# Kernel optimization log

Measured on AMD Instinct MI355X. Metric: run time of the kernel, lower is better.

Reference implementation:

```python
import jax, jax.numpy as jnp
import numpy as np


def setup_inputs() -> dict:
    key = jax.random.key(0)
    ks = jax.random.split(key, 8)
    N, D, DC, H, C = 100000, 1024, 512, 256, 2  # instances, feat, compressed, hidden, classes
    s = lambda k, sh: jax.random.normal(k, sh, dtype=jnp.float32) * 0.02
    return {
        "x": jax.random.normal(ks[0], (N, D), dtype=jnp.float32),
        "Wc": s(ks[1], (D, DC)), "bc": jnp.zeros((DC,), jnp.float32),
        "W1": s(ks[2], (D, H)), "b1": jnp.zeros((H,), jnp.float32),
        "W2": s(ks[3], (D, H)), "b2": jnp.zeros((H,), jnp.float32),
        "W3": s(ks[4], (H, C)), "b3": jnp.zeros((C,), jnp.float32),
        "Wbag": s(ks[5], (DC, 1)), "bbag": jnp.zeros((1,), jnp.float32),
        "Wins": s(ks[6], (DC, C)), "bins": jnp.zeros((C,), jnp.float32),
        "bag_label": 1,
        "n_ins": 8,
    }


def reference(x, Wc, bc, W1, b1, W2, b2, W3, b3, Wbag, bbag, Wins, bins, bag_label, n_ins):
    # G_Att_Net: compression + gated attention (vectorized over the per-instance loop)
    h = jax.nn.relu(x @ Wc + bc)                                  # [N, 512]
    a = jnp.tanh(x @ W1 + b1) * jax.nn.sigmoid(x @ W2 + b2)       # [N, 256] gated
    A = a @ W3 + b3                                               # [N, n_class]

    # Bag.h_slide: sum_i A[i]^T @ h[i]  ==  A^T @ h
    slide_agg_rep = A.T @ h                                       # [n_class, 512]
    slide_score_unnorm = (slide_agg_rep @ Wbag + bbag).reshape(1, -1)  # [1, n_class]
    Y_prob = jax.nn.softmax(slide_score_unnorm, axis=-1)
    Y_hat = jnp.argmax(slide_score_unnorm, axis=-1)

    # Ins.in_call: top-k positive / negative instances on attention column bag_label
    A_I = A[:, bag_label]                                         # [N]
    _, pos_idx = jax.lax.top_k(A_I, n_ins)
    _, neg_idx = jax.lax.top_k(-A_I, n_ins)
    ins_in = h[jnp.concatenate([pos_idx, neg_idx])]               # [2*n_ins, 512]
    ins_logits = jax.nn.softmax(ins_in @ Wins + bins, axis=-1)    # [2*n_ins, n_class]
    ins_labels = jnp.concatenate([jnp.ones((n_ins,), jnp.int32),
                                  jnp.zeros((n_ins,), jnp.int32)])
    return slide_score_unnorm, Y_hat, Y_prob, ins_logits, ins_labels
```

## Files before the change

### kernel.cpp

```cpp
#include <hip/hip_runtime.h>
#include <hip/hip_bf16.h>
#include <math.h>

typedef __attribute__((ext_vector_type(8))) short bf16x8;
typedef __attribute__((ext_vector_type(4))) float f32x4;

#define M_ROWS 100000
#define NBLK   1563

static __device__ __forceinline__ unsigned short f2bf(float f) {
  union { float f; unsigned u; } cv; cv.f = f;
  unsigned u = cv.u;
  return (unsigned short)((u + 0x7fffu + ((u >> 16) & 1u)) >> 16);
}

static __device__ __forceinline__ f32x4 mfma16(bf16x8 a, bf16x8 b, f32x4 c) {
  return __builtin_amdgcn_mfma_f32_16x16x32_bf16(a, b, c, 0, 0, 0);
}

static __device__ __forceinline__ void gload_lds16(const unsigned short* g, unsigned short* l) {
  __builtin_amdgcn_global_load_lds((const __attribute__((address_space(1))) unsigned int*)g,
                                   (__attribute__((address_space(3))) unsigned int*)l, 16, 0, 0);
}

__global__ void prep_kernel(const float* __restrict__ Wc, const float* __restrict__ W1,
                            const float* __restrict__ W2,
                            unsigned short* __restrict__ Wct, unsigned short* __restrict__ W1t,
                            unsigned short* __restrict__ W2t, float* __restrict__ agg1) {
  int i = blockIdx.x * blockDim.x + threadIdx.x;
  if (i < 1024) agg1[i] = 0.0f;
  if (i < 512 * 1024) {
    int c = i >> 10, k = i & 1023;
    Wct[i] = f2bf(Wc[k * 512 + c]);
  } else if (i < 768 * 1024) {
    int j = i - 512 * 1024;
    int c = j >> 10, k = j & 1023;
    W1t[j] = f2bf(W1[k * 256 + c]);
  } else if (i < 1024 * 1024) {
    int j = i - 768 * 1024;
    int c = j >> 10, k = j & 1023;
    W2t[j] = f2bf(W2[k * 256 + c]);
  }
}

__launch_bounds__(512)
__global__ void kernelA(const float* __restrict__ x,
                        const unsigned short* __restrict__ W1t, const unsigned short* __restrict__ W2t,
                        const float* __restrict__ b1, const float* __restrict__ b2,
                        const float* __restrict__ W3, const float* __restrict__ b3,
                        float* __restrict__ Ag) {
  __shared__ unsigned short xl[64 * 32];
  __shared__ unsigned short w1l[256 * 32];
  __shared__ unsigned short w2l[256 * 32];
  __shared__ float Alds[64 * 2];

  const int tid = threadIdx.x;
  const int lane = tid & 63, wid = tid >> 6;
  const int wm = wid >> 2, wj = wid & 3;
  const int lr = lane & 15, lg = lane >> 4;
  const int m0 = blockIdx.x * 64;

  f32x4 acc1[2][4], acc2[2][4];
#pragma unroll
  for (int m = 0; m < 2; m++)
#pragma unroll
    for (int n = 0; n < 4; n++) {
      acc1[m][n] = (f32x4){0.f, 0.f, 0.f, 0.f};
      acc2[m][n] = (f32x4){0.f, 0.f, 0.f, 0.f};
    }

  const int xr = tid >> 3;
  const bool xvalid = (m0 + xr) < M_ROWS;
  const float* xsrc = x + (size_t)(m0 + xr) * 1024 + ((tid & 7) << 2);
  unsigned short* xdst = &xl[tid * 4];

  const unsigned short* w1base = W1t + (size_t)(wid * 16 + (lane >> 2)) * 1024 + ((lane & 3) << 3);
  const unsigned short* w2base = W2t + (size_t)(wid * 16 + (lane >> 2)) * 1024 + ((lane & 3) << 3);
  unsigned short* w1dst0 = &w1l[wid * 512];
  unsigned short* w1dst1 = &w1l[4096 + wid * 512];
  unsigned short* w2dst0 = &w2l[wid * 512];
  unsigned short* w2dst1 = &w2l[4096 + wid * 512];

  const bf16x8* ap0 = (const bf16x8*)&xl[(wm * 32 + 0 + lr) * 32 + lg * 8];
  const bf16x8* ap1 = (const bf16x8*)&xl[(wm * 32 + 16 + lr) * 32 + lg * 8];
  const bf16x8* b1p[4]; const bf16x8* b2p[4];
#pragma unroll
  for (int n = 0; n < 4; n++) {
    b1p[n] = (const bf16x8*)&w1l[(wj * 64 + n * 16 + lr) * 32 + lg * 8];
    b2p[n] = (const bf16x8*)&w2l[(wj * 64 + n * 16 + lr) * 32 + lg * 8];
  }

  for (int ks = 0; ks < 32; ks++) {
    const int k0 = ks * 32;
    gload_lds16(w1base + k0, w1dst0);
    gload_lds16(w1base + 131072 + k0, w1dst1);
    gload_lds16(w2base + k0, w2dst0);
    gload_lds16(w2base + 131072 + k0, w2dst1);
    float4 xv = make_float4(0.f, 0.f, 0.f, 0.f);
    if (xvalid) xv = *(const float4*)(xsrc + k0);
    ushort4 xb;
    xb.x = f2bf(xv.x); xb.y = f2bf(xv.y); xb.z = f2bf(xv.z); xb.w = f2bf(xv.w);
    *(ushort4*)xdst = xb;
    __syncthreads();
    bf16x8 a0 = *ap0, a1 = *ap1;
#pragma unroll
    for (int n = 0; n < 4; n++) {
      bf16x8 bb1 = *b1p[n];
      acc1[0][n] = mfma16(a0, bb1, acc1[0][n]);
      acc1[1][n] = mfma16(a1, bb1, acc1[1][n]);
      bf16x8 bb2 = *b2p[n];
      acc2[0][n] = mfma16(a0, bb2, acc2[0][n]);
      acc2[1][n] = mfma16(a1, bb2, acc2[1][n]);
    }
    __syncthreads();
  }

  float pA[2][4][2];
#pragma unroll
  for (int m = 0; m < 2; m++)
#pragma unroll
    for (int r = 0; r < 4; r++) { pA[m][r][0] = 0.f; pA[m][r][1] = 0.f; }

#pragma unroll
  for (int n = 0; n < 4; n++) {
    const int j = wj * 64 + n * 16 + lr;
    const float bb1 = b1[j], bb2 = b2[j];
    const float w30 = W3[j * 2], w31 = W3[j * 2 + 1];
#pragma unroll
    for (int m = 0; m < 2; m++)
#pragma unroll
      for (int r = 0; r < 4; r++) {
        float u1 = acc1[m][n][r] + bb1;
        float u2 = acc2[m][n][r] + bb2;
        float av = tanhf(u1) * (1.0f / (1.0f + __expf(-u2)));
        pA[m][r][0] += av * w30;
        pA[m][r][1] += av * w31;
      }
  }
#pragma unroll
  for (int off = 1; off < 16; off <<= 1)
#pragma unroll
    for (int m = 0; m < 2; m++)
#pragma unroll
      for (int r = 0; r < 4; r++) {
        pA[m][r][0] += __shfl_xor(pA[m][r][0], off, 64);
        pA[m][r][1] += __shfl_xor(pA[m][r][1], off, 64);
      }

  if (tid < 128) Alds[tid] = 0.0f;
  __syncthreads();
  if (lr == 0) {
#pragma unroll
    for (int m = 0; m < 2; m++)
#pragma unroll
      for (int r = 0; r < 4; r++) {
        int row = wm * 32 + m * 16 + lg * 4 + r;
        atomicAdd(&Alds[row * 2 + 0], pA[m][r][0]);
        atomicAdd(&Alds[row * 2 + 1], pA[m][r][1]);
      }
  }
  __syncthreads();
  if (tid < 128) {
    int row = tid >> 1, c = tid & 1;
    if (m0 + row < M_ROWS) Ag[(size_t)(m0 + row) * 2 + c] = Alds[tid] + b3[c];
  }
}

template <bool MIN>
static __device__ __forceinline__ bool better(float v1, int i1, float v2, int i2) {
  if (MIN) return (v1 < v2) || (v1 == v2 && i1 < i2);
  else     return (v1 > v2) || (v1 == v2 && i1 < i2);
}

template <bool MIN>
static __device__ __forceinline__ void merge_lists(float* vL, int* iL, int t, int s) {
  float av[8], ov[8], mv[8];
  int ai[8], oi[8], mi[8];
#pragma unroll
  for (int p = 0; p < 8; p++) {
    av[p] = vL[t * 8 + p];       ai[p] = iL[t * 8 + p];
    ov[p] = vL[(t + s) * 8 + p]; oi[p] = iL[(t + s) * 8 + p];
  }
#pragma unroll
  for (int p = 0; p < 8; p++) {
    bool b = better<MIN>(av[p], ai[p], ov[7 - p], oi[7 - p]);
    mv[p] = b ? av[p] : ov[7 - p];
    mi[p] = b ? ai[p] : oi[7 - p];
  }
#define CE(i, j)                                                             \
  { if (!better<MIN>(mv[i], mi[i], mv[j], mi[j])) {                          \
      float tv = mv[i]; mv[i] = mv[j]; mv[j] = tv;                           \
      int tii = mi[i]; mi[i] = mi[j]; mi[j] = tii; } }
  CE(0, 4) CE(1, 5) CE(2, 6) CE(3, 7)
  CE(0, 2) CE(1, 3) CE(4, 6) CE(5, 7)
  CE(0, 1) CE(2, 3) CE(4, 5) CE(6, 7)
#undef CE
#pragma unroll
  for (int p = 0; p < 8; p++) { vL[t * 8 + p] = mv[p]; iL[t * 8 + p] = mi[p]; }
}

__launch_bounds__(256)
__global__ void topk_p1(const float* __restrict__ Ag, const int* __restrict__ bag_label,
                        float* __restrict__ tkv, int* __restrict__ tki,
                        float* __restrict__ bkv, int* __restrict__ bki) {
  __shared__ float tvL[256 * 8]; __shared__ int tiL[256 * 8];
  __shared__ float bvL[256 * 8]; __shared__ int biL[256 * 8];
  const int t = threadIdx.x;
  const int lab = bag_label[0];
  float tv[8], bv[8]; int ti[8], bi[8];
#pragma unroll
  for (int p = 0; p < 8; p++) {
    tv[p] = -3.4e38f; ti[p] = 0x7fffffff;
    bv[p] =  3.4e38f; bi[p] = 0x7fffffff;
  }
  for (int r = blockIdx.x * 256 + t; r < M_ROWS; r += 65536) {
    float v = Ag[(size_t)r * 2 + lab];
    {
      float cv = v; int ci = r;
#pragma unroll
      for (int p = 0; p < 8; p++) {
        bool b = (cv > tv[p]) || (cv == tv[p] && ci < ti[p]);
        if (b) { float t0 = tv[p]; int t1 = ti[p]; tv[p] = cv; ti[p] = ci; cv = t0; ci = t1; }
      }
    }
    {
      float cv = v; int ci = r;
#pragma unroll
      for (int p = 0; p < 8; p++) {
        bool b = (cv < bv[p]) || (cv == bv[p] && ci < bi[p]);
        if (b) { float t0 = bv[p]; int t1 = bi[p]; bv[p] = cv; bi[p] = ci; cv = t0; ci = t1; }
      }
    }
  }
#pragma unroll
  for (int p = 0; p < 8; p++) {
    tvL[t * 8 + p] = tv[p]; tiL[t * 8 + p] = ti[p];
    bvL[t * 8 + p] = bv[p]; biL[t * 8 + p] = bi[p];
  }
  __syncthreads();
  for (int s = 128; s > 0; s >>= 1) {
    if (t < s) {
      merge_lists<false>(tvL, tiL, t, s);
      merge_lists<true>(bvL, biL, t, s);
    }
    __syncthreads();
  }
  if (t < 8) {
    tkv[blockIdx.x * 8 + t] = tvL[t]; tki[blockIdx.x * 8 + t] = tiL[t];
    bkv[blockIdx.x * 8 + t] = bvL[t]; bki[blockIdx.x * 8 + t] = biL[t];
  }
}

__launch_bounds__(256)
__global__ void topk_p2(const float* __restrict__ tkv, const int* __restrict__ tki,
                        const float* __restrict__ bkv, const int* __restrict__ bki,
                        int* __restrict__ idxout, float* __restrict__ out) {
  __shared__ float tvL[256 * 8]; __shared__ int tiL[256 * 8];
  __shared__ float bvL[256 * 8]; __shared__ int biL[256 * 8];
  const int t = threadIdx.x;
#pragma unroll
  for (int p = 0; p < 8; p++) {
    tvL[t * 8 + p] = tkv[t * 8 + p]; tiL[t * 8 + p] = tki[t * 8 + p];
    bvL[t * 8 + p] = bkv[t * 8 + p]; biL[t * 8 + p] = bki[t * 8 + p];
  }
  __syncthreads();
  for (int s = 128; s > 0; s >>= 1) {
    if (t < s) {
      merge_lists<false>(tvL, tiL, t, s);
      merge_lists<true>(bvL, biL, t, s);
    }
    __syncthreads();
  }
  if (t == 0) {
#pragma unroll
    for (int p = 0; p < 8; p++) {
      idxout[p] = tiL[p];
      idxout[8 + p] = biL[p];
      out[37 + p] = 1.0f;
      out[45 + p] = 0.0f;
    }
  }
}

__launch_bounds__(512)
__global__ void kernelH(const float* __restrict__ x,
                        const unsigned short* __restrict__ Wct,
                        const float* __restrict__ bc,
                        const float* __restrict__ Ag,
                        const int* __restrict__ idx,
                        float* __restrict__ aggP,
                        float* __restrict__ hsel) {
  __shared__ unsigned short xl[64 * 32];
  __shared__ unsigned short wl[512 * 32];
  __shared__ float aggL[1024];
  __shared__ int selr[16];

  const int tid = threadIdx.x;
  const int lane = tid & 63, wid = tid >> 6;
  const int wm = wid >> 2, wc = wid & 3;
  const int lr = lane & 15, lg = lane >> 4;
  const int m0 = blockIdx.x * 64;

  f32x4 acc[2][8];
#pragma unroll
  for (int m = 0; m < 2; m++)
#pragma unroll
    for (int n = 0; n < 8; n++) acc[m][n] = (f32x4){0.f, 0.f, 0.f, 0.f};

  const int xr = tid >> 3;
  const bool xvalid = (m0 + xr) < M_ROWS;
  const float* xsrc = x + (size_t)(m0 + xr) * 1024 + ((tid & 7) << 2);
  unsigned short* xdst = &xl[tid * 4];

  const unsigned short* wbase = Wct + (size_t)(wid * 16 + (lane >> 2)) * 1024 + ((lane & 3) << 3);
  unsigned short* wdst0 = &wl[wid * 512];
  unsigned short* wdst1 = &wl[4096 + wid * 512];
  unsigned short* wdst2 = &wl[8192 + wid * 512];
  unsigned short* wdst3 = &wl[12288 + wid * 512];

  const bf16x8* ap0 = (const bf16x8*)&xl[(wm * 32 + 0 + lr) * 32 + lg * 8];
  const bf16x8* ap1 = (const bf16x8*)&xl[(wm * 32 + 16 + lr) * 32 + lg * 8];
  const bf16x8* bp[8];
#pragma unroll
  for (int n = 0; n < 8; n++)
    bp[n] = (const bf16x8*)&wl[(wc * 128 + n * 16 + lr) * 32 + lg * 8];

  for (int ks = 0; ks < 32; ks++) {
    const int k0 = ks * 32;
    gload_lds16(wbase + k0, wdst0);
    gload_lds16(wbase + 131072 + k0, wdst1);
    gload_lds16(wbase + 262144 + k0, wdst2);
    gload_lds16(wbase + 393216 + k0, wdst3);
    float4 xv = make_float4(0.f, 0.f, 0.f, 0.f);
    if (xvalid) xv = *(const float4*)(xsrc + k0);
    ushort4 xb;
    xb.x = f2bf(xv.x); xb.y = f2bf(xv.y); xb.z = f2bf(xv.z); xb.w = f2bf(xv.w);
    *(ushort4*)xdst = xb;
    __syncthreads();
    bf16x8 a0 = *ap0, a1 = *ap1;
#pragma unroll
    for (int n = 0; n < 8; n++) {
      bf16x8 bb = *bp[n];
      acc[0][n] = mfma16(a0, bb, acc[0][n]);
      acc[1][n] = mfma16(a1, bb, acc[1][n]);
    }
    __syncthreads();
  }

  if (tid < 16) {
    int r = idx[tid];
    selr[tid] = (r >= m0 && r < m0 + 64) ? (r - m0) : -1;
  }
  aggL[tid] = 0.0f;
  aggL[tid + 512] = 0.0f;
  __syncthreads();

  float av[2][4][2];
#pragma unroll
  for (int m = 0; m < 2; m++)
#pragma unroll
    for (int r = 0; r < 4; r++) {
      int row = m0 + wm * 32 + m * 16 + lg * 4 + r;
      bool valid = row < M_ROWS;
      av[m][r][0] = valid ? Ag[(size_t)row * 2 + 0] : 0.f;
      av[m][r][1] = valid ? Ag[(size_t)row * 2 + 1] : 0.f;
    }

  float contrib[8][2];
#pragma unroll
  for (int n = 0; n < 8; n++) { contrib[n][0] = 0.f; contrib[n][1] = 0.f; }

#pragma unroll
  for (int n = 0; n < 8; n++) {
    const float bcv = bc[wc * 128 + n * 16 + lr];
#pragma unroll
    for (int m = 0; m < 2; m++)
#pragma unroll
      for (int r = 0; r < 4; r++) {
        float h = fmaxf(acc[m][n][r] + bcv, 0.0f);
        acc[m][n][r] = h;
        contrib[n][0] += av[m][r][0] * h;
        contrib[n][1] += av[m][r][1] * h;
      }
  }
#pragma unroll
  for (int n = 0; n < 8; n++)
#pragma unroll
    for (int c = 0; c < 2; c++) {
      contrib[n][c] += __shfl_xor(contrib[n][c], 16, 64);
      contrib[n][c] += __shfl_xor(contrib[n][c], 32, 64);
    }
  if (lg == 0) {
#pragma unroll
    for (int n = 0; n < 8; n++) {
      atomicAdd(&aggL[wc * 128 + n * 16 + lr], contrib[n][0]);
      atomicAdd(&aggL[512 + wc * 128 + n * 16 + lr], contrib[n][1]);
    }
  }
#pragma unroll
  for (int s = 0; s < 16; s++) {
    int rl = selr[s];
    if (rl < 0 || (rl >> 5) != wm) continue;
#pragma unroll
    for (int m = 0; m < 2; m++)
#pragma unroll
      for (int r = 0; r < 4; r++)
        if (rl == wm * 32 + m * 16 + lg * 4 + r) {
#pragma unroll
          for (int n = 0; n < 8; n++)
            hsel[s * 512 + wc * 128 + n * 16 + lr] = acc[m][n][r];
        }
  }
  __syncthreads();
  aggP[(size_t)blockIdx.x * 1024 + tid] = aggL[tid];
  aggP[(size_t)blockIdx.x * 1024 + 512 + tid] = aggL[tid + 512];
}

__launch_bounds__(256)
__global__ void reduce_kernel(const float* __restrict__ aggP, float* __restrict__ agg1) {
  int tcol = (blockIdx.x & 3) * 256 + threadIdx.x;
  int g = blockIdx.x >> 2;
  int b0 = g * 98, b1 = min(NBLK, b0 + 98);
  float s = 0.f;
  for (int b = b0; b < b1; b++) s += aggP[(size_t)b * 1024 + tcol];
  atomicAdd(&agg1[tcol], s);
}

__launch_bounds__(1024)
__global__ void score_kernel(const float* __restrict__ agg1, const float* __restrict__ Wbag,
                             const float* __restrict__ bbag, float* __restrict__ out) {
  __shared__ float red[1024];
  int t = threadIdx.x;
  red[t] = agg1[t] * Wbag[t & 511];
  __syncthreads();
  for (int off = 256; off > 0; off >>= 1) {
    if ((t & 511) < off) red[t] += red[t + off];
    __syncthreads();
  }
  if (t == 0) {
    float s0 = red[0] + bbag[0];
    float s1 = red[512] + bbag[0];
    out[0] = s0; out[1] = s1;
    out[2] = (s1 > s0) ? 1.0f : 0.0f;
    float mx = fmaxf(s0, s1);
    float e0 = __expf(s0 - mx), e1 = __expf(s1 - mx);
    out[3] = e0 / (e0 + e1);
    out[4] = e1 / (e0 + e1);
  }
}

__launch_bounds__(512)
__global__ void ins_kernel(const float* __restrict__ hsel, const float* __restrict__ Wins,
                           const float* __restrict__ bins, float* __restrict__ out) {
  int lane = threadIdx.x & 63;
  int w = threadIdx.x >> 6;
#pragma unroll
  for (int si = 0; si < 2; si++) {
    int s = w * 2 + si;
    float z0 = 0.f, z1 = 0.f;
#pragma unroll
    for (int q = 0; q < 8; q++) {
      int c = lane * 8 + q;
      float h = hsel[s * 512 + c];
      z0 += h * Wins[c * 2 + 0];
      z1 += h * Wins[c * 2 + 1];
    }
#pragma unroll
    for (int off = 1; off < 64; off <<= 1) {
      z0 += __shfl_xor(z0, off, 64);
      z1 += __shfl_xor(z1, off, 64);
    }
    if (lane == 0) {
      z0 += bins[0]; z1 += bins[1];
      float mx = fmaxf(z0, z1);
      float e0 = __expf(z0 - mx), e1 = __expf(z1 - mx);
      float d = e0 + e1;
      out[5 + s * 2 + 0] = e0 / d;
      out[5 + s * 2 + 1] = e1 / d;
    }
  }
}

extern "C" void kernel_launch(void* const* d_in, const int* in_sizes, int n_in,
                              void* d_out, int out_size, void* d_ws, size_t ws_size,
                              hipStream_t stream) {
  (void)in_sizes; (void)n_in; (void)out_size; (void)ws_size;
  const float* x    = (const float*)d_in[0];
  const float* Wc   = (const float*)d_in[1];
  const float* bc   = (const float*)d_in[2];
  const float* W1   = (const float*)d_in[3];
  const float* b1   = (const float*)d_in[4];
  const float* W2   = (const float*)d_in[5];
  const float* b2   = (const float*)d_in[6];
  const float* W3   = (const float*)d_in[7];
  const float* b3   = (const float*)d_in[8];
  const float* Wbag = (const float*)d_in[9];
  const float* bbag = (const float*)d_in[10];
  const float* Wins = (const float*)d_in[11];
  const float* bins = (const float*)d_in[12];
  const int* bag_label = (const int*)d_in[13];
  float* out = (float*)d_out;
  char* ws = (char*)d_ws;

  unsigned short* Wct = (unsigned short*)(ws);
  unsigned short* W1t = (unsigned short*)(ws + 1048576);
  unsigned short* W2t = (unsigned short*)(ws + 1572864);
  float* Ag   = (float*)(ws + 2097152);
  float* aggP = (float*)(ws + 2897152);
  int*   idx  = (int*)  (ws + 9299200);
  float* hsel = (float*)(ws + 9299264);
  float* agg1 = (float*)(ws + 9332032);
  float* tkv  = (float*)(ws + 9336128);
  int*   tki  = (int*)  (ws + 9344320);
  float* bkv  = (float*)(ws + 9352512);
  int*   bki  = (int*)  (ws + 9360704);

  prep_kernel<<<4096, 256, 0, stream>>>(Wc, W1, W2, Wct, W1t, W2t, agg1);
  kernelA<<<NBLK, 512, 0, stream>>>(x, W1t, W2t, b1, b2, W3, b3, Ag);
  topk_p1<<<256, 256, 0, stream>>>(Ag, bag_label, tkv, tki, bkv, bki);
  topk_p2<<<1, 256, 0, stream>>>(tkv, tki, bkv, bki, idx, out);
  kernelH<<<NBLK, 512, 0, stream>>>(x, Wct, bc, Ag, idx, aggP, hsel);
  reduce_kernel<<<64, 256, 0, stream>>>(aggP, agg1);
  score_kernel<<<1, 1024, 0, stream>>>(agg1, Wbag, bbag, out);
  ins_kernel<<<1, 512, 0, stream>>>(hsel, Wins, bins, out);
}
```

Before: 1.049 ms.

## Retile both GEMMs into 128x128 N-split blocks and recompute selected rows separately

Both projection GEMMs now use 128-row by 128-column tiles on a 2D grid that splits the output columns across blocks, in place of one block covering all columns for 64 rows. W1 and W2 are interleaved into a single packed weight so each attention block holds matching tanh and sigmoid columns, and partial attention scores are combined with global atomics into an Ag buffer pre-seeded with b3. The selected top-k rows of h are recomputed by a small dedicated kernel, so the main GEMM no longer scans for them. The trade-off is that x is now read and converted four times per GEMM, once per column block, and A is accumulated with global atomics.

```diff
diff --git a/kernel.cpp b/kernel.cpp
--- a/kernel.cpp
+++ b/kernel.cpp
@@ -4,15 +4,19 @@
 
 typedef __attribute__((ext_vector_type(8))) short bf16x8;
 typedef __attribute__((ext_vector_type(4))) float f32x4;
+typedef __attribute__((ext_vector_type(8))) unsigned short u16x8;
 
 #define M_ROWS 100000
-#define NBLK   1563
+#define MBLK   782
 
 static __device__ __forceinline__ unsigned short f2bf(float f) {
   union { float f; unsigned u; } cv; cv.f = f;
   unsigned u = cv.u;
   return (unsigned short)((u + 0x7fffu + ((u >> 16) & 1u)) >> 16);
 }
+static __device__ __forceinline__ float bf2f(unsigned short u) {
+  union { unsigned u; float f; } cv; cv.u = ((unsigned)u) << 16; return cv.f;
+}
 
 static __device__ __forceinline__ f32x4 mfma16(bf16x8 a, bf16x8 b, f32x4 c) {
   return __builtin_amdgcn_mfma_f32_16x16x32_bf16(a, b, c, 0, 0, 0);
@@ -24,93 +28,87 @@
 }
 
 __global__ void prep_kernel(const float* __restrict__ Wc, const float* __restrict__ W1,
-                            const float* __restrict__ W2,
-                            unsigned short* __restrict__ Wct, unsigned short* __restrict__ W1t,
-                            unsigned short* __restrict__ W2t, float* __restrict__ agg1) {
+                            const float* __restrict__ W2, const float* __restrict__ b3,
+                            unsigned short* __restrict__ Wct, unsigned short* __restrict__ Wat,
+                            float* __restrict__ Ag, float* __restrict__ agg1) {
   int i = blockIdx.x * blockDim.x + threadIdx.x;
-  if (i < 1024) agg1[i] = 0.0f;
-  if (i < 512 * 1024) {
+  if (i < 524288) {
     int c = i >> 10, k = i & 1023;
     Wct[i] = f2bf(Wc[k * 512 + c]);
-  } else if (i < 768 * 1024) {
-    int j = i - 512 * 1024;
-    int c = j >> 10, k = j & 1023;
-    W1t[j] = f2bf(W1[k * 256 + c]);
-  } else if (i < 1024 * 1024) {
-    int j = i - 768 * 1024;
-    int c = j >> 10, k = j & 1023;
-    W2t[j] = f2bf(W2[k * 256 + c]);
-  }
-}
-
-__launch_bounds__(512)
-__global__ void kernelA(const float* __restrict__ x,
-                        const unsigned short* __restrict__ W1t, const unsigned short* __restrict__ W2t,
-                        const float* __restrict__ b1, const float* __restrict__ b2,
-                        const float* __restrict__ W3, const float* __restrict__ b3,
-                        float* __restrict__ Ag) {
-  __shared__ unsigned short xl[64 * 32];
-  __shared__ unsigned short w1l[256 * 32];
-  __shared__ unsigned short w2l[256 * 32];
-  __shared__ float Alds[64 * 2];
+  } else if (i < 1048576) {
+    int j = i - 524288;
+    int g = j >> 10, k = j & 1023;
+    int nb = g >> 7, cc = g & 127;
+    float v = (cc < 64) ? W1[k * 256 + nb * 64 + cc] : W2[k * 256 + nb * 64 + cc - 64];
+    Wat[j] = f2bf(v);
+  } else if (i < 1248576) {
+    int i2 = i - 1048576;
+    Ag[i2] = b3[i2 & 1];
+  } else if (i < 1249600) {
+    agg1[i - 1248576] = 0.0f;
+  }
+}
+
+__launch_bounds__(256)
+__global__ void gemmA(const float* __restrict__ x, const unsigned short* __restrict__ Wat,
+                      const float* __restrict__ b1, const float* __restrict__ b2,
+                      const float* __restrict__ W3, float* __restrict__ Ag) {
+  __shared__ unsigned short xl[128 * 32];
+  __shared__ unsigned short wl[128 * 32];
 
   const int tid = threadIdx.x;
-  const int lane = tid & 63, wid = tid >> 6;
-  const int wm = wid >> 2, wj = wid & 3;
+  const int lane = tid & 63, w = tid >> 6;
   const int lr = lane & 15, lg = lane >> 4;
-  const int m0 = blockIdx.x * 64;
-
-  f32x4 acc1[2][4], acc2[2][4];
+  const int nb = blockIdx.x;
+  const int m0 = blockIdx.y * 128;
+
+  f32x4 acc[2][8];
 #pragma unroll
   for (int m = 0; m < 2; m++)
 #pragma unroll
-    for (int n = 0; n < 4; n++) {
-      acc1[m][n] = (f32x4){0.f, 0.f, 0.f, 0.f};
-      acc2[m][n] = (f32x4){0.f, 0.f, 0.f, 0.f};
-    }
-
-  const int xr = tid >> 3;
+    for (int n = 0; n < 8; n++) acc[m][n] = (f32x4){0.f, 0.f, 0.f, 0.f};
+
+  const int xr = tid >> 1;
   const bool xvalid = (m0 + xr) < M_ROWS;
-  const float* xsrc = x + (size_t)(m0 + xr) * 1024 + ((tid & 7) << 2);
-  unsigned short* xdst = &xl[tid * 4];
-
-  const unsigned short* w1base = W1t + (size_t)(wid * 16 + (lane >> 2)) * 1024 + ((lane & 3) << 3);
-  const unsigned short* w2base = W2t + (size_t)(wid * 16 + (lane >> 2)) * 1024 + ((lane & 3) << 3);
-  unsigned short* w1dst0 = &w1l[wid * 512];
-  unsigned short* w1dst1 = &w1l[4096 + wid * 512];
-  unsigned short* w2dst0 = &w2l[wid * 512];
-  unsigned short* w2dst1 = &w2l[4096 + wid * 512];
-
-  const bf16x8* ap0 = (const bf16x8*)&xl[(wm * 32 + 0 + lr) * 32 + lg * 8];
-  const bf16x8* ap1 = (const bf16x8*)&xl[(wm * 32 + 16 + lr) * 32 + lg * 8];
-  const bf16x8* b1p[4]; const bf16x8* b2p[4];
-#pragma unroll
-  for (int n = 0; n < 4; n++) {
-    b1p[n] = (const bf16x8*)&w1l[(wj * 64 + n * 16 + lr) * 32 + lg * 8];
-    b2p[n] = (const bf16x8*)&w2l[(wj * 64 + n * 16 + lr) * 32 + lg * 8];
-  }
+  const float* xsrc = x + (size_t)(m0 + xr) * 1024 + ((tid & 1) << 4);
+  unsigned short* xdst = &xl[xr * 32 + ((tid & 1) << 4)];
+
+  const unsigned short* wsrc0 = Wat + ((size_t)nb * 128 + w * 32 + (lane >> 2)) * 1024 + ((lane & 3) << 3);
+  const unsigned short* wsrc1 = wsrc0 + (size_t)16 * 1024;
+  unsigned short* wdst0 = &wl[w * 1024];
+  unsigned short* wdst1 = &wl[w * 1024 + 512];
+
+  const bf16x8* ap0 = (const bf16x8*)&xl[(w * 32 + lr) * 32 + lg * 8];
+  const bf16x8* ap1 = (const bf16x8*)&xl[(w * 32 + 16 + lr) * 32 + lg * 8];
+  const bf16x8* bp[8];
+#pragma unroll
+  for (int n = 0; n < 8; n++) bp[n] = (const bf16x8*)&wl[(n * 16 + lr) * 32 + lg * 8];
 
   for (int ks = 0; ks < 32; ks++) {
     const int k0 = ks * 32;
-    gload_lds16(w1base + k0, w1dst0);
-    gload_lds16(w1base + 131072 + k0, w1dst1);
-    gload_lds16(w2base + k0, w2dst0);
-    gload_lds16(w2base + 131072 + k0, w2dst1);
-    float4 xv = make_float4(0.f, 0.f, 0.f, 0.f);
-    if (xvalid) xv = *(const float4*)(xsrc + k0);
-    ushort4 xb;
-    xb.x = f2bf(xv.x); xb.y = f2bf(xv.y); xb.z = f2bf(xv.z); xb.w = f2bf(xv.w);
-    *(ushort4*)xdst = xb;
+    gload_lds16(wsrc0 + k0, wdst0);
+    gload_lds16(wsrc1 + k0, wdst1);
+    float4 v0 = make_float4(0.f,0.f,0.f,0.f), v1 = v0, v2 = v0, v3 = v0;
+    if (xvalid) {
+      v0 = *(const float4*)(xsrc + k0);
+      v1 = *(const float4*)(xsrc + k0 + 4);
+      v2 = *(const float4*)(xsrc + k0 + 8);
+      v3 = *(const float4*)(xsrc + k0 + 12);
+    }
+    u16x8 pa, pb;
+    pa[0]=f2bf(v0.x); pa[1]=f2bf(v0.y); pa[2]=f2bf(v0.z); pa[3]=f2bf(v0.w);
+    pa[4]=f2bf(v1.x); pa[5]=f2bf(v1.y); pa[6]=f2bf(v1.z); pa[7]=f2bf(v1.w);
+    pb[0]=f2bf(v2.x); pb[1]=f2bf(v2.y); pb[2]=f2bf(v2.z); pb[3]=f2bf(v2.w);
+    pb[4]=f2bf(v3.x); pb[5]=f2bf(v3.y); pb[6]=f2bf(v3.z); pb[7]=f2bf(v3.w);
+    *(u16x8*)xdst = pa;
+    *(u16x8*)(xdst + 8) = pb;
     __syncthreads();
     bf16x8 a0 = *ap0, a1 = *ap1;
 #pragma unroll
-    for (int n = 0; n < 4; n++) {
-      bf16x8 bb1 = *b1p[n];
-      acc1[0][n] = mfma16(a0, bb1, acc1[0][n]);
-      acc1[1][n] = mfma16(a1, bb1, acc1[1][n]);
-      bf16x8 bb2 = *b2p[n];
-      acc2[0][n] = mfma16(a0, bb2, acc2[0][n]);
-      acc2[1][n] = mfma16(a1, bb2, acc2[1][n]);
+    for (int n = 0; n < 8; n++) {
+      bf16x8 bb = *bp[n];
+      acc[0][n] = mfma16(a0, bb, acc[0][n]);
+      acc[1][n] = mfma16(a1, bb, acc[1][n]);
     }
     __syncthreads();
   }
@@ -123,15 +121,15 @@
 
 #pragma unroll
   for (int n = 0; n < 4; n++) {
-    const int j = wj * 64 + n * 16 + lr;
+    const int j = nb * 64 + n * 16 + lr;
     const float bb1 = b1[j], bb2 = b2[j];
     const float w30 = W3[j * 2], w31 = W3[j * 2 + 1];
 #pragma unroll
     for (int m = 0; m < 2; m++)
 #pragma unroll
       for (int r = 0; r < 4; r++) {
-        float u1 = acc1[m][n][r] + bb1;
-        float u2 = acc2[m][n][r] + bb2;
+        float u1 = acc[m][n][r] + bb1;
+        float u2 = acc[m][n + 4][r] + bb2;
         float av = tanhf(u1) * (1.0f / (1.0f + __expf(-u2)));
         pA[m][r][0] += av * w30;
         pA[m][r][1] += av * w31;
@@ -146,24 +144,126 @@
         pA[m][r][0] += __shfl_xor(pA[m][r][0], off, 64);
         pA[m][r][1] += __shfl_xor(pA[m][r][1], off, 64);
       }
-
-  if (tid < 128) Alds[tid] = 0.0f;
+  if (lr == 0) {
+#pragma unroll
+    for (int m = 0; m < 2; m++)
+#pragma unroll
+      for (int r = 0; r < 4; r++) {
+        int row = m0 + w * 32 + m * 16 + lg * 4 + r;
+        if (row < M_ROWS) {
+          atomicAdd(&Ag[(size_t)row * 2 + 0], pA[m][r][0]);
+          atomicAdd(&Ag[(size_t)row * 2 + 1], pA[m][r][1]);
+        }
+      }
+  }
+}
+
+__launch_bounds__(256)
+__global__ void gemmH(const float* __restrict__ x, const unsigned short* __restrict__ Wct,
+                      const float* __restrict__ bc, const float* __restrict__ Ag,
+                      float* __restrict__ aggP) {
+  __shared__ unsigned short xl[128 * 32];
+  __shared__ unsigned short wl[128 * 32];
+  __shared__ float aggL[256];
+
+  const int tid = threadIdx.x;
+  const int lane = tid & 63, w = tid >> 6;
+  const int lr = lane & 15, lg = lane >> 4;
+  const int nb = blockIdx.x;
+  const int m0 = blockIdx.y * 128;
+
+  f32x4 acc[2][8];
+#pragma unroll
+  for (int m = 0; m < 2; m++)
+#pragma unroll
+    for (int n = 0; n < 8; n++) acc[m][n] = (f32x4){0.f, 0.f, 0.f, 0.f};
+
+  const int xr = tid >> 1;
+  const bool xvalid = (m0 + xr) < M_ROWS;
+  const float* xsrc = x + (size_t)(m0 + xr) * 1024 + ((tid & 1) << 4);
+  unsigned short* xdst = &xl[xr * 32 + ((tid & 1) << 4)];
+
+  const unsigned short* wsrc0 = Wct + ((size_t)nb * 128 + w * 32 + (lane >> 2)) * 1024 + ((lane & 3) << 3);
+  const unsigned short* wsrc1 = wsrc0 + (size_t)16 * 1024;
+  unsigned short* wdst0 = &wl[w * 1024];
+  unsigned short* wdst1 = &wl[w * 1024 + 512];
+
+  const bf16x8* ap0 = (const bf16x8*)&xl[(w * 32 + lr) * 32 + lg * 8];
+  const bf16x8* ap1 = (const bf16x8*)&xl[(w * 32 + 16 + lr) * 32 + lg * 8];
+  const bf16x8* bp[8];
+#pragma unroll
+  for (int n = 0; n < 8; n++) bp[n] = (const bf16x8*)&wl[(n * 16 + lr) * 32 + lg * 8];
+
+  for (int ks = 0; ks < 32; ks++) {
+    const int k0 = ks * 32;
+    gload_lds16(wsrc0 + k0, wdst0);
+    gload_lds16(wsrc1 + k0, wdst1);
+    float4 v0 = make_float4(0.f,0.f,0.f,0.f), v1 = v0, v2 = v0, v3 = v0;
+    if (xvalid) {
+      v0 = *(const float4*)(xsrc + k0);
+      v1 = *(const float4*)(xsrc + k0 + 4);
+      v2 = *(const float4*)(xsrc + k0 + 8);
+      v3 = *(const float4*)(xsrc + k0 + 12);
+    }
+    u16x8 pa, pb;
+    pa[0]=f2bf(v0.x); pa[1]=f2bf(v0.y); pa[2]=f2bf(v0.z); pa[3]=f2bf(v0.w);
+    pa[4]=f2bf(v1.x); pa[5]=f2bf(v1.y); pa[6]=f2bf(v1.z); pa[7]=f2bf(v1.w);
+    pb[0]=f2bf(v2.x); pb[1]=f2bf(v2.y); pb[2]=f2bf(v2.z); pb[3]=f2bf(v2.w);
+    pb[4]=f2bf(v3.x); pb[5]=f2bf(v3.y); pb[6]=f2bf(v3.z); pb[7]=f2bf(v3.w);
+    *(u16x8*)xdst = pa;
+    *(u16x8*)(xdst + 8) = pb;
+    __syncthreads();
+    bf16x8 a0 = *ap0, a1 = *ap1;
+#pragma unroll
+    for (int n = 0; n < 8; n++) {
+      bf16x8 bb = *bp[n];
+      acc[0][n] = mfma16(a0, bb, acc[0][n]);
+      acc[1][n] = mfma16(a1, bb, acc[1][n]);
+    }
+    __syncthreads();
+  }
+
+  float A0[2][4], A1[2][4];
+#pragma unroll
+  for (int m = 0; m < 2; m++)
+#pragma unroll
+    for (int r = 0; r < 4; r++) {
+      int row = m0 + w * 32 + m * 16 + lg * 4 + r;
+      bool valid = row < M_ROWS;
+      A0[m][r] = valid ? Ag[(size_t)row * 2 + 0] : 0.f;
+      A1[m][r] = valid ? Ag[(size_t)row * 2 + 1] : 0.f;
+    }
+  float c0[8], c1[8];
+#pragma unroll
+  for (int n = 0; n < 8; n++) { c0[n] = 0.f; c1[n] = 0.f; }
+#pragma unroll
+  for (int n = 0; n < 8; n++) {
+    const float bcv = bc[nb * 128 + n * 16 + lr];
+#pragma unroll
+    for (int m = 0; m < 2; m++)
+#pragma unroll
+      for (int r = 0; r < 4; r++) {
+        float h = fmaxf(acc[m][n][r] + bcv, 0.0f);
+        c0[n] += A0[m][r] * h;
+        c1[n] += A1[m][r] * h;
+      }
+  }
+#pragma unroll
+  for (int n = 0; n < 8; n++) {
+    c0[n] += __shfl_xor(c0[n], 16, 64); c0[n] += __shfl_xor(c0[n], 32, 64);
+    c1[n] += __shfl_xor(c1[n], 16, 64); c1[n] += __shfl_xor(c1[n], 32, 64);
+  }
+  aggL[tid] = 0.0f;
   __syncthreads();
-  if (lr == 0) {
-#pragma unroll
-    for (int m = 0; m < 2; m++)
-#pragma unroll
-      for (int r = 0; r < 4; r++) {
-        int row = wm * 32 + m * 16 + lg * 4 + r;
-        atomicAdd(&Alds[row * 2 + 0], pA[m][r][0]);
-        atomicAdd(&Alds[row * 2 + 1], pA[m][r][1]);
-      }
+  if (lane < 16) {
+#pragma unroll
+    for (int n = 0; n < 8; n++) {
+      atomicAdd(&aggL[(n * 16 + lane) * 2 + 0], c0[n]);
+      atomicAdd(&aggL[(n * 16 + lane) * 2 + 1], c1[n]);
+    }
   }
   __syncthreads();
-  if (tid < 128) {
-    int row = tid >> 1, c = tid & 1;
-    if (m0 + row < M_ROWS) Ag[(size_t)(m0 + row) * 2 + c] = Alds[tid] + b3[c];
-  }
+  aggP[(size_t)blockIdx.y * 1024 + nb * 256 + tid] = aggL[tid];
 }
 
 template <bool MIN>
@@ -282,164 +382,54 @@
   }
 }
 
-__launch_bounds__(512)
-__global__ void kernelH(const float* __restrict__ x,
-                        const unsigned short* __restrict__ Wct,
-                        const float* __restrict__ bc,
-                        const float* __restrict__ Ag,
-                        const int* __restrict__ idx,
-                        float* __restrict__ aggP,
-                        float* __restrict__ hsel) {
-  __shared__ unsigned short xl[64 * 32];
-  __shared__ unsigned short wl[512 * 32];
-  __shared__ float aggL[1024];
-  __shared__ int selr[16];
-
-  const int tid = threadIdx.x;
-  const int lane = tid & 63, wid = tid >> 6;
-  const int wm = wid >> 2, wc = wid & 3;
-  const int lr = lane & 15, lg = lane >> 4;
-  const int m0 = blockIdx.x * 64;
-
-  f32x4 acc[2][8];
-#pragma unroll
-  for (int m = 0; m < 2; m++)
-#pragma unroll
-    for (int n = 0; n < 8; n++) acc[m][n] = (f32x4){0.f, 0.f, 0.f, 0.f};
-
-  const int xr = tid >> 3;
-  const bool xvalid = (m0 + xr) < M_ROWS;
-  const float* xsrc = x + (size_t)(m0 + xr) * 1024 + ((tid & 7) << 2);
-  unsigned short* xdst = &xl[tid * 4];
-
-  const unsigned short* wbase = Wct + (size_t)(wid * 16 + (lane >> 2)) * 1024 + ((lane & 3) << 3);
-  unsigned short* wdst0 = &wl[wid * 512];
-  unsigned short* wdst1 = &wl[4096 + wid * 512];
-  unsigned short* wdst2 = &wl[8192 + wid * 512];
-  unsigned short* wdst3 = &wl[12288 + wid * 512];
-
-  const bf16x8* ap0 = (const bf16x8*)&xl[(wm * 32 + 0 + lr) * 32 + lg * 8];
-  const bf16x8* ap1 = (const bf16x8*)&xl[(wm * 32 + 16 + lr) * 32 + lg * 8];
-  const bf16x8* bp[8];
-#pragma unroll
-  for (int n = 0; n < 8; n++)
-    bp[n] = (const bf16x8*)&wl[(wc * 128 + n * 16 + lr) * 32 + lg * 8];
-
-  for (int ks = 0; ks < 32; ks++) {
-    const int k0 = ks * 32;
-    gload_lds16(wbase + k0, wdst0);
-    gload_lds16(wbase + 131072 + k0, wdst1);
-    gload_lds16(wbase + 262144 + k0, wdst2);
-    gload_lds16(wbase + 393216 + k0, wdst3);
-    float4 xv = make_float4(0.f, 0.f, 0.f, 0.f);
-    if (xvalid) xv = *(const float4*)(xsrc + k0);
-    ushort4 xb;
-    xb.x = f2bf(xv.x); xb.y = f2bf(xv.y); xb.z = f2bf(xv.z); xb.w = f2bf(xv.w);
-    *(ushort4*)xdst = xb;
-    __syncthreads();
-    bf16x8 a0 = *ap0, a1 = *ap1;
-#pragma unroll
-    for (int n = 0; n < 8; n++) {
-      bf16x8 bb = *bp[n];
-      acc[0][n] = mfma16(a0, bb, acc[0][n]);
-      acc[1][n] = mfma16(a1, bb, acc[1][n]);
-    }
-    __syncthreads();
-  }
-
-  if (tid < 16) {
-    int r = idx[tid];
-    selr[tid] = (r >= m0 && r < m0 + 64) ? (r - m0) : -1;
-  }
-  aggL[tid] = 0.0f;
-  aggL[tid + 512] = 0.0f;
+__launch_bounds__(256)
+__global__ void hsel_kernel(const float* __restrict__ x, const unsigned short* __restrict__ Wct,
+                            const float* __restrict__ bc, const int* __restrict__ idx,
+                            float* __restrict__ hsel) {
+  __shared__ float xrow[1024];
+  const int t = threadIdx.x;
+  const int r = idx[blockIdx.x];
+  *(float4*)&xrow[t * 4] = *(const float4*)(x + (size_t)r * 1024 + t * 4);
   __syncthreads();
-
-  float av[2][4][2];
-#pragma unroll
-  for (int m = 0; m < 2; m++)
-#pragma unroll
-    for (int r = 0; r < 4; r++) {
-      int row = m0 + wm * 32 + m * 16 + lg * 4 + r;
-      bool valid = row < M_ROWS;
-      av[m][r][0] = valid ? Ag[(size_t)row * 2 + 0] : 0.f;
-      av[m][r][1] = valid ? Ag[(size_t)row * 2 + 1] : 0.f;
-    }
-
-  float contrib[8][2];
-#pragma unroll
-  for (int n = 0; n < 8; n++) { contrib[n][0] = 0.f; contrib[n][1] = 0.f; }
-
-#pragma unroll
-  for (int n = 0; n < 8; n++) {
-    const float bcv = bc[wc * 128 + n * 16 + lr];
-#pragma unroll
-    for (int m = 0; m < 2; m++)
-#pragma unroll
-      for (int r = 0; r < 4; r++) {
-        float h = fmaxf(acc[m][n][r] + bcv, 0.0f);
-        acc[m][n][r] = h;
-        contrib[n][0] += av[m][r][0] * h;
-        contrib[n][1] += av[m][r][1] * h;
-      }
-  }
-#pragma unroll
-  for (int n = 0; n < 8; n++)
-#pragma unroll
-    for (int c = 0; c < 2; c++) {
-      contrib[n][c] += __shfl_xor(contrib[n][c], 16, 64);
-      contrib[n][c] += __shfl_xor(contrib[n][c], 32, 64);
-    }
-  if (lg == 0) {
-#pragma unroll
-    for (int n = 0; n < 8; n++) {
-      atomicAdd(&aggL[wc * 128 + n * 16 + lr], contrib[n][0]);
-      atomicAdd(&aggL[512 + wc * 128 + n * 16 + lr], contrib[n][1]);
-    }
-  }
-#pragma unroll
-  for (int s = 0; s < 16; s++) {
-    int rl = selr[s];
-    if (rl < 0 || (rl >> 5) != wm) continue;
-#pragma unroll
-    for (int m = 0; m < 2; m++)
-#pragma unroll
-      for (int r = 0; r < 4; r++)
-        if (rl == wm * 32 + m * 16 + lg * 4 + r) {
-#pragma unroll
-          for (int n = 0; n < 8; n++)
-            hsel[s * 512 + wc * 128 + n * 16 + lr] = acc[m][n][r];
-        }
-  }
-  __syncthreads();
-  aggP[(size_t)blockIdx.x * 1024 + tid] = aggL[tid];
-  aggP[(size_t)blockIdx.x * 1024 + 512 + tid] = aggL[tid + 512];
+#pragma unroll
+  for (int half = 0; half < 2; half++) {
+    int c = t + half * 256;
+    float s = 0.f;
+    for (int k = 0; k < 1024; k += 8) {
+      u16x8 w8 = *(const u16x8*)&Wct[(size_t)c * 1024 + k];
+#pragma unroll
+      for (int q = 0; q < 8; q++) s += bf2f(w8[q]) * xrow[k + q];
+    }
+    hsel[blockIdx.x * 512 + c] = fmaxf(s + bc[c], 0.0f);
+  }
 }
 
 __launch_bounds__(256)
 __global__ void reduce_kernel(const float* __restrict__ aggP, float* __restrict__ agg1) {
-  int tcol = (blockIdx.x & 3) * 256 + threadIdx.x;
-  int g = blockIdx.x >> 2;
-  int b0 = g * 98, b1 = min(NBLK, b0 + 98);
+  int flat = (blockIdx.x & 3) * 256 + threadIdx.x;
+  int mg = blockIdx.x >> 2;
+  int b0 = mg * 98, b1 = min(MBLK, b0 + 98);
   float s = 0.f;
-  for (int b = b0; b < b1; b++) s += aggP[(size_t)b * 1024 + tcol];
-  atomicAdd(&agg1[tcol], s);
-}
-
-__launch_bounds__(1024)
+  for (int b = b0; b < b1; b++) s += aggP[(size_t)b * 1024 + flat];
+  atomicAdd(&agg1[flat], s);
+}
+
+__launch_bounds__(512)
 __global__ void score_kernel(const float* __restrict__ agg1, const float* __restrict__ Wbag,
                              const float* __restrict__ bbag, float* __restrict__ out) {
-  __shared__ float red[1024];
+  __shared__ float r0[512], r1[512];
   int t = threadIdx.x;
-  red[t] = agg1[t] * Wbag[t & 511];
+  float wb = Wbag[t];
+  r0[t] = agg1[t * 2 + 0] * wb;
+  r1[t] = agg1[t * 2 + 1] * wb;
   __syncthreads();
   for (int off = 256; off > 0; off >>= 1) {
-    if ((t & 511) < off) red[t] += red[t + off];
+    if (t < off) { r0[t] += r0[t + off]; r1[t] += r1[t + off]; }
     __syncthreads();
   }
   if (t == 0) {
-    float s0 = red[0] + bbag[0];
-    float s1 = red[512] + bbag[0];
+    float s0 = r0[0] + bbag[0];
+    float s1 = r1[0] + bbag[0];
     out[0] = s0; out[1] = s1;
     out[2] = (s1 > s0) ? 1.0f : 0.0f;
     float mx = fmaxf(s0, s1);
@@ -503,24 +493,24 @@
   char* ws = (char*)d_ws;
 
   unsigned short* Wct = (unsigned short*)(ws);
-  unsigned short* W1t = (unsigned short*)(ws + 1048576);
-  unsigned short* W2t = (unsigned short*)(ws + 1572864);
+  unsigned short* Wat = (unsigned short*)(ws + 1048576);
   float* Ag   = (float*)(ws + 2097152);
   float* aggP = (float*)(ws + 2897152);
-  int*   idx  = (int*)  (ws + 9299200);
-  float* hsel = (float*)(ws + 9299264);
-  float* agg1 = (float*)(ws + 9332032);
-  float* tkv  = (float*)(ws + 9336128);
-  int*   tki  = (int*)  (ws + 9344320);
-  float* bkv  = (float*)(ws + 9352512);
-  int*   bki  = (int*)  (ws + 9360704);
-
-  prep_kernel<<<4096, 256, 0, stream>>>(Wc, W1, W2, Wct, W1t, W2t, agg1);
-  kernelA<<<NBLK, 512, 0, stream>>>(x, W1t, W2t, b1, b2, W3, b3, Ag);
+  float* agg1 = (float*)(ws + 6100224);
+  int*   idx  = (int*)  (ws + 6104320);
+  float* hsel = (float*)(ws + 6104384);
+  float* tkv  = (float*)(ws + 6137152);
+  int*   tki  = (int*)  (ws + 6145344);
+  float* bkv  = (float*)(ws + 6153536);
+  int*   bki  = (int*)  (ws + 6161728);
+
+  prep_kernel<<<4882, 256, 0, stream>>>(Wc, W1, W2, b3, Wct, Wat, Ag, agg1);
+  gemmA<<<dim3(4, MBLK), 256, 0, stream>>>(x, Wat, b1, b2, W3, Ag);
   topk_p1<<<256, 256, 0, stream>>>(Ag, bag_label, tkv, tki, bkv, bki);
   topk_p2<<<1, 256, 0, stream>>>(tkv, tki, bkv, bki, idx, out);
-  kernelH<<<NBLK, 512, 0, stream>>>(x, Wct, bc, Ag, idx, aggP, hsel);
-  reduce_kernel<<<64, 256, 0, stream>>>(aggP, agg1);
-  score_kernel<<<1, 1024, 0, stream>>>(agg1, Wbag, bbag, out);
+  gemmH<<<dim3(4, MBLK), 256, 0, stream>>>(x, Wct, bc, Ag, aggP);
+  hsel_kernel<<<16, 256, 0, stream>>>(x, Wct, bc, idx, hsel);
+  reduce_kernel<<<32, 256, 0, stream>>>(aggP, agg1);
+  score_kernel<<<1, 512, 0, stream>>>(agg1, Wbag, bbag, out);
   ins_kernel<<<1, 512, 0, stream>>>(hsel, Wins, bins, out);
 }
```

Result: slower. 1.194 ms (+13.8%).
